# Kernel optimization log

Measured on AMD Instinct MI355X. Metric: run time of the kernel, lower is better.

## Reference

```python
import jax, jax.numpy as jnp
import numpy as np
import math
from jax import lax

STRIDES = (8.0, 16.0, 32.0)
ANCHORS = (
    ((6.1, 8.1), (20.6, 12.6), (11.2, 23.7)),
    ((36.2, 26.8), (25.9, 57.2), (57.8, 47.9)),
    ((122.1, 78.3), (73.7, 143.8), (236.1, 213.1)),
)
NUM_CLASSES = 80
L = NUM_CLASSES + 5
NA = 3
SCORE_T = 0.1
NMS_T = 0.6
DETECTIONS = 100
TOPK = 1000          # static cap on post-threshold candidates per image
IMG = 640            # batched image H=W; also max_size used for class offsets


def setup_inputs() -> dict:
    key = jax.random.key(0)
    ks = jax.random.split(key, 8)
    N = 8
    chans = (128, 256, 512)
    hw = (80, 40, 20)
    inp = {}
    for i, (c, s) in enumerate(zip(chans, hw)):
        inp[f"f{i}"] = jax.random.normal(ks[i], (N, c, s, s), jnp.float32)
        inp[f"w{i}"] = jax.random.normal(ks[3 + i], (NA * L, c), jnp.float32) * 0.02
        b = np.zeros((NA, L), np.float32)
        b[:, 4] += math.log(8 / (416 / STRIDES[i]) ** 2)   # Predictor bias init
        b[:, 5:] += math.log(0.6 / (NUM_CLASSES - 0.99))
        inp[f"b{i}"] = jnp.asarray(b.reshape(-1))
    inp["scale_factors"] = jnp.ones((N,), jnp.float32)
    return inp


def _decode_level(f, w, b, stride, anchors):
    # f: [N,Cin,H,W]; w: [NA*L,Cin]; 1x1 conv == channel GEMM
    N, _, H, W = f.shape
    p = jnp.einsum('nchw,oc->nhwo', f, w) + b
    p = jax.nn.sigmoid(p.reshape(N, H, W, NA, L))
    gx, gy = jnp.meshgrid(jnp.arange(W, dtype=f.dtype), jnp.arange(H, dtype=f.dtype), indexing='xy')
    grid = jnp.stack((gx, gy), axis=-1)                       # [H,W,2] (x,y)
    xy = (2 * p[..., :2] - 0.5 + grid[None, :, :, None, :]) * stride
    wh = 4 * p[..., 2:4] ** 2 * anchors[None, None, None, :, :]
    box = jnp.concatenate((xy, wh), axis=-1).reshape(N, -1, 4)
    obj = p[..., 4].reshape(N, -1)
    cls = p[..., 5:].reshape(N, -1, NUM_CLASSES)
    return box, obj, cls


def _cxcywh2xyxy(b):
    cx, cy, w, h = b[..., 0], b[..., 1], b[..., 2], b[..., 3]
    return jnp.stack((cx - w / 2, cy - h / 2, cx + w / 2, cy + h / 2), axis=-1)


def _iou_one_many(b, boxes):
    lt = jnp.maximum(b[:2], boxes[:, :2])
    rb = jnp.minimum(b[2:], boxes[:, 2:])
    wh = jnp.clip(rb - lt, 0)
    inter = wh[:, 0] * wh[:, 1]
    area_b = (b[2] - b[0]) * (b[3] - b[1])
    areas = (boxes[:, 2] - boxes[:, 0]) * (boxes[:, 3] - boxes[:, 1])
    return inter / (area_b + areas - inter + 1e-7)


def _nms_fixed(boxes, scores):
    # greedy NMS, fixed DETECTIONS iterations; boxes already class-offset
    def step(valid, _):
        s = jnp.where(valid, scores, -jnp.inf)
        i = jnp.argmax(s)
        ok = s[i] > 0.0
        ious = _iou_one_many(boxes[i], boxes)
        nv = valid & (ious <= NMS_T)
        nv = nv.at[i].set(False)
        valid = jnp.where(ok, nv, valid)
        return valid, (jnp.where(ok, i, -1), ok)

    valid0 = scores > SCORE_T
    _, (idx, ok) = lax.scan(step, valid0, None, length=DETECTIONS)
    return idx, ok


def _per_image(boxes, obj, cls, sf):
    scores = obj[:, None] * cls                               # [A,C]
    mask = (obj[:, None] > SCORE_T) & (scores > SCORE_T)
    scores = jnp.where(mask, scores, -1.0)
    topv, topi = lax.top_k(scores.reshape(-1), TOPK)
    anchor = topi // NUM_CLASSES
    label = topi % NUM_CLASSES
    cb = boxes[anchor]
    cb = jnp.clip(cb, 0.0, float(IMG))                        # image_shapes = (IMG, IMG)
    off = cb + (label * IMG).astype(cb.dtype)[:, None]        # batched_nms class offset
    idx, ok = _nms_fixed(off, topv)
    gi = jnp.clip(idx, 0)
    okf = ok.astype(cb.dtype)
    out_box = cb[gi] / sf * okf[:, None]
    out_score = topv[gi] * okf
    out_label = label[gi].astype(cb.dtype) * okf
    return jnp.concatenate((out_box, out_score[:, None], out_label[:, None]), axis=1)  # [DET,6]


def reference(f0, f1, f2, w0, b0, w1, b1, w2, b2, scale_factors):
    feats = (f0, f1, f2)
    ws = (w0, w1, w2)
    bs = (b0, b1, b2)
    boxes, objs, clss = [], [], []
    for i in range(3):
        a = jnp.asarray(ANCHORS[i], dtype=f0.dtype)
        bx, ob, cl = _decode_level(feats[i], ws[i], bs[i], STRIDES[i], a)
        boxes.append(bx)
        objs.append(ob)
        clss.append(cl)
    boxes = _cxcywh2xyxy(jnp.concatenate(boxes, axis=1))      # [N, 25200, 4]
    obj = jnp.concatenate(objs, axis=1)                       # [N, 25200]
    cls = jnp.concatenate(clss, axis=1)                       # [N, 25200, 80]
    return jax.vmap(_per_image)(boxes, obj, cls, scale_factors)  # [N, DET, 6]
```

## Files before the change

kernel.cpp:

```cpp
#include <hip/hip_runtime.h>
#include <math.h>


#define IMG_F 640.0f

#define WT_F     0
#define N_WT     344064
#define WT_L0    0
#define WT_L1    49152
#define WT_L2    147456
#define CAND_F   344064
#define CAP1     4096
#define CNT_F    (CAND_F + CAP1*2)
#define IMGBUF_F (CNT_F + 16)
#define CAP2     2048

#define LOGIT_T (-2.1972245773362196f)

__constant__ float d_anch[3][3][2] = {
  {{6.1f,8.1f},{20.6f,12.6f},{11.2f,23.7f}},
  {{36.2f,26.8f},{25.9f,57.2f},{57.8f,47.9f}},
  {{122.1f,78.3f},{73.7f,143.8f},{236.1f,213.1f}},
};
__constant__ float d_stridec[3] = {8.f,16.f,32.f};

__global__ __launch_bounds__(256) void ka_init(
    float* __restrict__ ws, float* __restrict__ out,
    const float* __restrict__ w0, const float* __restrict__ w1,
    const float* __restrict__ w2) {
  int i = blockIdx.x * 256 + threadIdx.x;
  if (i < 4800) out[i] = 0.f;
  if (i < 16)   ((int*)ws)[CNT_F + i] = 0;
  if (i < N_WT) {
    int C, i2; const float* w;
    if (i < WT_L1)      { C = 128; i2 = i;         w = w0; }
    else if (i < WT_L2) { C = 256; i2 = i - WT_L1; w = w1; }
    else                { C = 512; i2 = i - WT_L2; w = w2; }
    int a = i2 / (C * 128);
    int r = i2 - a * (C * 128);
    int c = r >> 7, l = r & 127;
    ws[WT_F + i] = (l < 85) ? w[(size_t)(a * 85 + l) * C + c] : 0.f;
  }
}

__global__ __launch_bounds__(256) void kb_obj(
    const float* __restrict__ f0, const float* __restrict__ f1,
    const float* __restrict__ f2,
    const float* __restrict__ w0, const float* __restrict__ w1,
    const float* __restrict__ w2,
    const float* __restrict__ b0, const float* __restrict__ b1,
    const float* __restrict__ b2, float* __restrict__ ws) {
  __shared__ float red[3104];
  int b = blockIdx.x, t = threadIdx.x;
  int level, Q, lq, S, bq0, C, HW;
  const float *f, *w, *bb;
  if (b < 400)      { level = 0; Q = 32; lq = 5; S = 8;  bq0 = b * 32;         C = 128; HW = 6400; f = f0; w = w0; bb = b0; }
  else if (b < 600) { level = 1; Q = 16; lq = 4; S = 16; bq0 = (b - 400) * 16; C = 256; HW = 1600; f = f1; w = w1; bb = b1; }
  else              { level = 2; Q = 8;  lq = 3; S = 32; bq0 = (b - 600) * 8;  C = 512; HW = 400;  f = f2; w = w2; bb = b2; }
  int q = t & (Q - 1), sl = t >> lq;
  int qpi = HW >> 2;
  int gq = bq0 + q;
  int n = gq / qpi;
  int sq = (gq - n * qpi) << 2;
  int kbase = sl * 16;
  const float* fp = f + ((size_t)(n * C + kbase)) * HW + sq;
  const float* wp = w + 4 * C + kbase;
  float acc[3][4] = {{0.f,0.f,0.f,0.f},{0.f,0.f,0.f,0.f},{0.f,0.f,0.f,0.f}};
  #pragma unroll
  for (int c = 0; c < 16; ++c) {
    float4 v = *(const float4*)(fp + (size_t)c * HW);
    float wa0 = wp[c];
    float wa1 = wp[85 * C + c];
    float wa2 = wp[170 * C + c];
    acc[0][0] = fmaf(v.x, wa0, acc[0][0]); acc[0][1] = fmaf(v.y, wa0, acc[0][1]);
    acc[0][2] = fmaf(v.z, wa0, acc[0][2]); acc[0][3] = fmaf(v.w, wa0, acc[0][3]);
    acc[1][0] = fmaf(v.x, wa1, acc[1][0]); acc[1][1] = fmaf(v.y, wa1, acc[1][1]);
    acc[1][2] = fmaf(v.z, wa1, acc[1][2]); acc[1][3] = fmaf(v.w, wa1, acc[1][3]);
    acc[2][0] = fmaf(v.x, wa2, acc[2][0]); acc[2][1] = fmaf(v.y, wa2, acc[2][1]);
    acc[2][2] = fmaf(v.z, wa2, acc[2][2]); acc[2][3] = fmaf(v.w, wa2, acc[2][3]);
  }
  int stride = Q * 12 + 1;
  int base = sl * stride + q * 12;
  #pragma unroll
  for (int a = 0; a < 3; ++a)
    #pragma unroll
    for (int p = 0; p < 4; ++p)
      red[base + a * 4 + p] = acc[a][p];
  __syncthreads();
  for (int r = t; r < Q * 12; r += 256) {
    int qq = r / 12, ap = r - qq * 12;
    int a = ap >> 2, p = ap & 3;
    float sum = 0.f;
    for (int s2 = 0; s2 < S; ++s2) sum += red[s2 * stride + qq * 12 + ap];
    float logit = sum + bb[a * 85 + 4];
    if (logit > LOGIT_T) {
      float obj = 1.f / (1.f + expf(-logit));
      int gq2 = bq0 + qq;
      int n2 = gq2 / qpi;
      int s = ((gq2 - n2 * qpi) << 2) + p;
      int idx = atomicAdd((int*)ws + CNT_F, 1);
      if (idx < CAP1) {
        int* cd = (int*)ws + CAND_F + idx * 2;
        cd[0] = (n2 << 24) | (level << 20) | (a << 16) | s;
        ((float*)cd)[1] = obj;
      }
    }
  }
}

template<int C, int HW, int Wd>
__device__ __forceinline__ void kc_cand(
    int level, int n, int a, int s, float obj,
    const float* __restrict__ f, const float* __restrict__ wTl,
    const float* __restrict__ bb, float* __restrict__ ws,
    float* __restrict__ fc, int lane) {
  #pragma unroll
  for (int j = 0; j < C / 64; ++j)
    fc[lane + 64 * j] = f[((size_t)(n * C + lane + 64 * j)) * HW + s];
  const float* wA = wTl + (size_t)a * C * 128;
  float acc1 = 0.f, acc2 = 0.f;
  #pragma unroll 8
  for (int c = 0; c < C; ++c) {
    float fv = fc[c];
    const float* wl = wA + c * 128;
    acc1 = fmaf(fv, wl[lane], acc1);
    acc2 = fmaf(fv, wl[64 + lane], acc2);
  }
  acc1 += bb[a * 85 + lane];
  float sig1 = 1.f / (1.f + expf(-acc1));
  float sig2 = 0.f;
  if (lane < 21) {
    acc2 += bb[a * 85 + 64 + lane];
    sig2 = 1.f / (1.f + expf(-acc2));
  }
  float p0 = __shfl(sig1, 0, 64), p1 = __shfl(sig1, 1, 64);
  float p2 = __shfl(sig1, 2, 64), p3 = __shfl(sig1, 3, 64);
  int gx = s % Wd, gy = s / Wd;
  float st = d_stridec[level];
  float cx = (2.f * p0 - 0.5f + (float)gx) * st;
  float cy = (2.f * p1 - 0.5f + (float)gy) * st;
  float bw = 4.f * p2 * p2 * d_anch[level][a][0];
  float bh = 4.f * p3 * p3 * d_anch[level][a][1];
  float x1 = fminf(fmaxf(cx - bw * 0.5f, 0.f), IMG_F);
  float y1 = fminf(fmaxf(cy - bh * 0.5f, 0.f), IMG_F);
  float x2 = fminf(fmaxf(cx + bw * 0.5f, 0.f), IMG_F);
  float y2 = fminf(fmaxf(cy + bh * 0.5f, 0.f), IMG_F);
  #pragma unroll
  for (int half = 0; half < 2; ++half) {
    bool on = half == 0 ? (lane >= 5) : (lane < 21);
    float sc = obj * (half == 0 ? sig1 : sig2);
    int cls = half == 0 ? (lane - 5) : (59 + lane);
    if (on && sc > 0.1f) {
      int p = atomicAdd((int*)ws + CNT_F + 1 + n, 1);
      if (p < CAP2) {
        float* dst = ws + IMGBUF_F + ((size_t)(n * CAP2 + p)) * 6;
        dst[0] = x1; dst[1] = y1; dst[2] = x2; dst[3] = y2;
        dst[4] = sc; dst[5] = (float)cls;
      }
    }
  }
}

__global__ __launch_bounds__(256) void kc_score(
    const float* __restrict__ f0, const float* __restrict__ f1,
    const float* __restrict__ f2,
    const float* __restrict__ b0, const float* __restrict__ b1,
    const float* __restrict__ b2, float* __restrict__ ws) {
  __shared__ float fcol[4][512];
  int wv = threadIdx.x >> 6, lane = threadIdx.x & 63;
  int count = min(((int*)ws)[CNT_F], CAP1);
  int nslots = gridDim.x * 4;
  for (int cid = blockIdx.x * 4 + wv; cid < count; cid += nslots) {
    int* cd = (int*)ws + CAND_F + cid * 2;
    int code = cd[0]; float obj = ((float*)cd)[1];
    int n = code >> 24, level = (code >> 20) & 15, a = (code >> 16) & 3, s = code & 0xFFFF;
    if (level == 0)
      kc_cand<128, 6400, 80>(0, n, a, s, obj, f0, ws + WT_F + WT_L0, b0, ws, fcol[wv], lane);
    else if (level == 1)
      kc_cand<256, 1600, 40>(1, n, a, s, obj, f1, ws + WT_F + WT_L1, b1, ws, fcol[wv], lane);
    else
      kc_cand<512, 400, 20>(2, n, a, s, obj, f2, ws + WT_F + WT_L2, b2, ws, fcol[wv], lane);
  }
}

__global__ __launch_bounds__(256) void kd_nms(
    const float* __restrict__ ws, float* __restrict__ out,
    const float* __restrict__ sfp) {
  __shared__ float bx1[CAP2], by1[CAP2], bx2[CAP2], by2[CAP2], bsc[CAP2], blb[CAP2];
  __shared__ int bval[CAP2];
  __shared__ float rs[256];
  __shared__ int ri[256];
  int n = blockIdx.x, tid = threadIdx.x;
  int cnt = min(((const int*)ws)[CNT_F + 1 + n], CAP2);
  for (int i = tid; i < cnt; i += 256) {
    const float* src = ws + IMGBUF_F + ((size_t)(n * CAP2 + i)) * 6;
    bx1[i] = src[0]; by1[i] = src[1]; bx2[i] = src[2]; by2[i] = src[3];
    bsc[i] = src[4]; blb[i] = src[5]; bval[i] = 1;
  }
  __syncthreads();
  float sf = sfp[n];
  for (int it = 0; it < 100; ++it) {
    float best = -1.f; int bi = -1;
    for (int i = tid; i < cnt; i += 256)
      if (bval[i] && bsc[i] > best) { best = bsc[i]; bi = i; }
    rs[tid] = best; ri[tid] = bi;
    __syncthreads();
    for (int off = 128; off > 0; off >>= 1) {
      if (tid < off && rs[tid + off] > rs[tid]) { rs[tid] = rs[tid + off]; ri[tid] = ri[tid + off]; }
      __syncthreads();
    }
    int wi = ri[0]; float wsc = rs[0];
    if (wi < 0) break;
    if (tid == 0) {
      float* o = out + (size_t)(n * 100 + it) * 6;
      o[0] = bx1[wi] / sf; o[1] = by1[wi] / sf;
      o[2] = bx2[wi] / sf; o[3] = by2[wi] / sf;
      o[4] = wsc;          o[5] = blb[wi];
    }
    float ofw = blb[wi] * IMG_F;
    float wx1 = bx1[wi] + ofw, wy1 = by1[wi] + ofw;
    float wx2 = bx2[wi] + ofw, wy2 = by2[wi] + ofw;
    float wa = (wx2 - wx1) * (wy2 - wy1);
    for (int i = tid; i < cnt; i += 256) {
      if (bval[i]) {
        float o2 = blb[i] * IMG_F;
        float x1 = bx1[i] + o2, y1 = by1[i] + o2, x2 = bx2[i] + o2, y2 = by2[i] + o2;
        float iw = fmaxf(fminf(wx2, x2) - fmaxf(wx1, x1), 0.f);
        float ih = fmaxf(fminf(wy2, y2) - fmaxf(wy1, y1), 0.f);
        float inter = iw * ih;
        float area = (x2 - x1) * (y2 - y1);
        float iou = inter / (wa + area - inter + 1e-7f);
        if (iou > 0.6f) bval[i] = 0;
      }
    }
    if (tid == 0) bval[wi] = 0;
    __syncthreads();
  }
}

extern "C" void kernel_launch(void* const* d_in, const int* in_sizes, int n_in,
                              void* d_out, int out_size, void* d_ws, size_t ws_size,
                              hipStream_t stream) {
  const float* f0 = (const float*)d_in[0];
  const float* w0 = (const float*)d_in[1];
  const float* b0 = (const float*)d_in[2];
  const float* f1 = (const float*)d_in[3];
  const float* w1 = (const float*)d_in[4];
  const float* b1 = (const float*)d_in[5];
  const float* f2 = (const float*)d_in[6];
  const float* w2 = (const float*)d_in[7];
  const float* b2 = (const float*)d_in[8];
  const float* sf = (const float*)d_in[9];
  float* out = (float*)d_out;
  float* ws  = (float*)d_ws;

  ka_init <<<1344, 256, 0, stream>>>(ws, out, w0, w1, w2);
  kb_obj  <<<700,  256, 0, stream>>>(f0, f1, f2, w0, w1, w2, b0, b1, b2, ws);
  kc_score<<<128,  256, 0, stream>>>(f0, f1, f2, b0, b1, b2, ws);
  kd_nms  <<<8,    256, 0, stream>>>(ws, out, sf);
}
```

Before: 130.1 us.

## Fold init kernel into objectness pass and use per-block candidate buckets

Removes the separate init kernel by moving the weight transpose and counter reset into kb_obj. Output zeroing now happens inside NMS, which clears only the unused rows. The global candidate atomic counter is replaced by a shared-memory counter per block, with each block writing its candidates to its own fixed bucket. kc_score walks these buckets instead of a single compacted list. The changes cut a launch and reduce global atomic contention, but each block is limited to 64 candidates and the work split in the scoring pass is uneven.

```diff
diff --git a/kernel.cpp b/kernel.cpp
--- a/kernel.cpp
+++ b/kernel.cpp
@@ -9,10 +9,11 @@
 #define WT_L0    0
 #define WT_L1    49152
 #define WT_L2    147456
-#define CAND_F   344064
-#define CAP1     4096
-#define CNT_F    (CAND_F + CAP1*2)
-#define IMGBUF_F (CNT_F + 16)
+#define CNTB_F   344064
+#define IMGCNT_F 344768
+#define NSLOT    64
+#define CANDB_F  344776
+#define IMGBUF_F (CANDB_F + 700 * NSLOT * 2)
 #define CAP2     2048
 
 #define LOGIT_T (-2.1972245773362196f)
@@ -24,14 +25,19 @@
 };
 __constant__ float d_stridec[3] = {8.f,16.f,32.f};
 
-__global__ __launch_bounds__(256) void ka_init(
-    float* __restrict__ ws, float* __restrict__ out,
+__global__ __launch_bounds__(256) void kb_obj(
+    const float* __restrict__ f0, const float* __restrict__ f1,
+    const float* __restrict__ f2,
     const float* __restrict__ w0, const float* __restrict__ w1,
-    const float* __restrict__ w2) {
-  int i = blockIdx.x * 256 + threadIdx.x;
-  if (i < 4800) out[i] = 0.f;
-  if (i < 16)   ((int*)ws)[CNT_F + i] = 0;
-  if (i < N_WT) {
+    const float* __restrict__ w2,
+    const float* __restrict__ b0, const float* __restrict__ b1,
+    const float* __restrict__ b2, float* __restrict__ ws) {
+  __shared__ float red[3104];
+  __shared__ int lcnt;
+  int b = blockIdx.x, t = threadIdx.x;
+  if (t == 0) lcnt = 0;
+  if (b == 0 && t < 8) ((int*)ws)[IMGCNT_F + t] = 0;
+  for (int i = b * 256 + t; i < N_WT; i += 700 * 256) {
     int C, i2; const float* w;
     if (i < WT_L1)      { C = 128; i2 = i;         w = w0; }
     else if (i < WT_L2) { C = 256; i2 = i - WT_L1; w = w1; }
@@ -41,17 +47,6 @@
     int c = r >> 7, l = r & 127;
     ws[WT_F + i] = (l < 85) ? w[(size_t)(a * 85 + l) * C + c] : 0.f;
   }
-}
-
-__global__ __launch_bounds__(256) void kb_obj(
-    const float* __restrict__ f0, const float* __restrict__ f1,
-    const float* __restrict__ f2,
-    const float* __restrict__ w0, const float* __restrict__ w1,
-    const float* __restrict__ w2,
-    const float* __restrict__ b0, const float* __restrict__ b1,
-    const float* __restrict__ b2, float* __restrict__ ws) {
-  __shared__ float red[3104];
-  int b = blockIdx.x, t = threadIdx.x;
   int level, Q, lq, S, bq0, C, HW;
   const float *f, *w, *bb;
   if (b < 400)      { level = 0; Q = 32; lq = 5; S = 8;  bq0 = b * 32;         C = 128; HW = 6400; f = f0; w = w0; bb = b0; }
@@ -98,14 +93,16 @@
       int gq2 = bq0 + qq;
       int n2 = gq2 / qpi;
       int s = ((gq2 - n2 * qpi) << 2) + p;
-      int idx = atomicAdd((int*)ws + CNT_F, 1);
-      if (idx < CAP1) {
-        int* cd = (int*)ws + CAND_F + idx * 2;
+      int idx = atomicAdd(&lcnt, 1);
+      if (idx < NSLOT) {
+        int* cd = (int*)ws + CANDB_F + (b * NSLOT + idx) * 2;
         cd[0] = (n2 << 24) | (level << 20) | (a << 16) | s;
         ((float*)cd)[1] = obj;
       }
     }
   }
+  __syncthreads();
+  if (t == 0) ((int*)ws)[CNTB_F + b] = min(lcnt, NSLOT);
 }
 
 template<int C, int HW, int Wd>
@@ -151,7 +148,7 @@
     float sc = obj * (half == 0 ? sig1 : sig2);
     int cls = half == 0 ? (lane - 5) : (59 + lane);
     if (on && sc > 0.1f) {
-      int p = atomicAdd((int*)ws + CNT_F + 1 + n, 1);
+      int p = atomicAdd((int*)ws + IMGCNT_F + n, 1);
       if (p < CAP2) {
         float* dst = ws + IMGBUF_F + ((size_t)(n * CAP2 + p)) * 6;
         dst[0] = x1; dst[1] = y1; dst[2] = x2; dst[3] = y2;
@@ -168,18 +165,21 @@
     const float* __restrict__ b2, float* __restrict__ ws) {
   __shared__ float fcol[4][512];
   int wv = threadIdx.x >> 6, lane = threadIdx.x & 63;
-  int count = min(((int*)ws)[CNT_F], CAP1);
-  int nslots = gridDim.x * 4;
-  for (int cid = blockIdx.x * 4 + wv; cid < count; cid += nslots) {
-    int* cd = (int*)ws + CAND_F + cid * 2;
-    int code = cd[0]; float obj = ((float*)cd)[1];
-    int n = code >> 24, level = (code >> 20) & 15, a = (code >> 16) & 3, s = code & 0xFFFF;
-    if (level == 0)
-      kc_cand<128, 6400, 80>(0, n, a, s, obj, f0, ws + WT_F + WT_L0, b0, ws, fcol[wv], lane);
-    else if (level == 1)
-      kc_cand<256, 1600, 40>(1, n, a, s, obj, f1, ws + WT_F + WT_L1, b1, ws, fcol[wv], lane);
-    else
-      kc_cand<512, 400, 20>(2, n, a, s, obj, f2, ws + WT_F + WT_L2, b2, ws, fcol[wv], lane);
+  int slot = blockIdx.x * 4 + wv;
+  int reg0 = slot >> 1, ph = slot & 1;
+  for (int reg = reg0; reg < 700; reg += 256) {
+    int cnt = min(((int*)ws)[CNTB_F + reg], NSLOT);
+    for (int ci = ph; ci < cnt; ci += 2) {
+      int* cd = (int*)ws + CANDB_F + (reg * NSLOT + ci) * 2;
+      int code = cd[0]; float obj = ((float*)cd)[1];
+      int n = code >> 24, level = (code >> 20) & 15, a = (code >> 16) & 3, s = code & 0xFFFF;
+      if (level == 0)
+        kc_cand<128, 6400, 80>(0, n, a, s, obj, f0, ws + WT_F + WT_L0, b0, ws, fcol[wv], lane);
+      else if (level == 1)
+        kc_cand<256, 1600, 40>(1, n, a, s, obj, f1, ws + WT_F + WT_L1, b1, ws, fcol[wv], lane);
+      else
+        kc_cand<512, 400, 20>(2, n, a, s, obj, f2, ws + WT_F + WT_L2, b2, ws, fcol[wv], lane);
+    }
   }
 }
 
@@ -191,7 +191,7 @@
   __shared__ float rs[256];
   __shared__ int ri[256];
   int n = blockIdx.x, tid = threadIdx.x;
-  int cnt = min(((const int*)ws)[CNT_F + 1 + n], CAP2);
+  int cnt = min(((const int*)ws)[IMGCNT_F + n], CAP2);
   for (int i = tid; i < cnt; i += 256) {
     const float* src = ws + IMGBUF_F + ((size_t)(n * CAP2 + i)) * 6;
     bx1[i] = src[0]; by1[i] = src[1]; bx2[i] = src[2]; by2[i] = src[3];
@@ -210,7 +210,11 @@
       __syncthreads();
     }
     int wi = ri[0]; float wsc = rs[0];
-    if (wi < 0) break;
+    if (wi < 0) {
+      for (int r2 = it * 6 + tid; r2 < 600; r2 += 256)
+        out[(size_t)n * 600 + r2] = 0.f;
+      break;
+    }
     if (tid == 0) {
       float* o = out + (size_t)(n * 100 + it) * 6;
       o[0] = bx1[wi] / sf; o[1] = by1[wi] / sf;
@@ -254,8 +258,7 @@
   float* out = (float*)d_out;
   float* ws  = (float*)d_ws;
 
-  ka_init <<<1344, 256, 0, stream>>>(ws, out, w0, w1, w2);
-  kb_obj  <<<700,  256, 0, stream>>>(f0, f1, f2, w0, w1, w2, b0, b1, b2, ws);
-  kc_score<<<128,  256, 0, stream>>>(f0, f1, f2, b0, b1, b2, ws);
-  kd_nms  <<<8,    256, 0, stream>>>(ws, out, sf);
-}
+  kb_obj  <<<700, 256, 0, stream>>>(f0, f1, f2, w0, w1, w2, b0, b1, b2, ws);
+  kc_score<<<128, 256, 0, stream>>>(f0, f1, f2, b0, b1, b2, ws);
+  kd_nms  <<<8,   256, 0, stream>>>(ws, out, sf);
+}
```

New measurement: 165.9 us. 1.28x slower.
